# Kernel tuning notes

Measured on AMD Instinct MI355X. Metric: run time of the kernel, lower is better.

## Reference

```python
import jax, jax.numpy as jnp
import numpy as np

N, C, H, W = 4, 256, 64, 64
C_EMBED = C // 2  # 128

def setup_inputs() -> dict:
    key = jax.random.key(0)
    k1, k2, k3, k4 = jax.random.split(key, 4)
    x = jax.random.normal(k1, (N, C, H, W), dtype=jnp.float32)
    # 1x1 conv weights stored as [out_ch, in_ch] (torch Conv2d weight squeezed)
    theta_w = jax.random.normal(k2, (C_EMBED, C), dtype=jnp.float32) * 0.01
    phi_w = jax.random.normal(k3, (C_EMBED, C), dtype=jnp.float32) * 0.01
    proj_w = jax.random.normal(k4, (C, C), dtype=jnp.float32) * 0.01
    return {"x": x, "theta_w": theta_w, "phi_w": phi_w, "proj_w": proj_w}

def reference(x, theta_w, phi_w, proj_w):
    n, c, h, w = x.shape
    s = h * w
    xf = x.reshape(n, c, s)  # [n, c, s]
    theta = jnp.einsum('ec,ncs->nse', theta_w, xf)  # [n, s, e]
    phi = jnp.einsum('ec,ncs->nes', phi_w, xf)      # [n, e, s]
    scale = jnp.sqrt(jnp.float32(theta_w.shape[0]))
    f = jnp.einsum('nse,net->nst', theta, phi) / scale  # [n, s, s]
    f = jax.nn.softmax(f, axis=-1)
    y = jnp.einsum('nst,nct->ncs', f, xf)  # attend over g = x, -> [n, c, s]
    res = jnp.einsum('oc,ncs->nos', proj_w, y)  # 1x1 projection conv
    return x + res.reshape(n, c, h, w)
```

## Files before the change

kernel.cpp:

```cpp
#include <hip/hip_runtime.h>
#include <cstdint>
#include <cstddef>

#define NB 4
#define CH 256
#define SS 4096
#define EE 128
#define QSCALE 0.08838834764831845f

typedef __attribute__((ext_vector_type(8))) short bfrag;
typedef __attribute__((ext_vector_type(8))) unsigned short u16x8;
typedef __attribute__((ext_vector_type(4))) float f32x4;

__device__ __forceinline__ unsigned short f2bf(float f) {
  union { float f; unsigned int u; } v; v.f = f;
  unsigned int u = v.u;
  unsigned int r = u + 0x7FFFu + ((u >> 16) & 1u);
  return (unsigned short)(r >> 16);
}

__global__ __launch_bounds__(256) void cvt_all(
    const float* __restrict__ x,   const float* __restrict__ thw,
    const float* __restrict__ phw, const float* __restrict__ pw,
    unsigned short* __restrict__ xb,   unsigned short* __restrict__ thwb,
    unsigned short* __restrict__ phwb, unsigned short* __restrict__ pwb)
{
  const int nx4 = NB * CH * SS / 4;
  const int nw4 = EE * CH / 4;
  const int np4 = CH * CH / 4;
  int i = blockIdx.x * 256 + threadIdx.x;
  const float* src; unsigned short* dst; int off;
  if      (i < nx4)                 { src = x;   dst = xb;   off = i; }
  else if (i < nx4 + nw4)           { src = thw; dst = thwb; off = i - nx4; }
  else if (i < nx4 + 2 * nw4)       { src = phw; dst = phwb; off = i - nx4 - nw4; }
  else if (i < nx4 + 2 * nw4 + np4) { src = pw;  dst = pwb;  off = i - nx4 - 2 * nw4; }
  else return;
  float4 v = reinterpret_cast<const float4*>(src)[off];
  ushort4 o;
  o.x = f2bf(v.x); o.y = f2bf(v.y); o.z = f2bf(v.z); o.w = f2bf(v.w);
  reinterpret_cast<ushort4*>(dst)[off] = o;
}

__global__ __launch_bounds__(256) void pass1_qk(
    const unsigned short* __restrict__ xb,
    const unsigned short* __restrict__ thw,
    const unsigned short* __restrict__ phw,
    unsigned short* __restrict__ Qt,
    unsigned short* __restrict__ Kt)
{
  __shared__ unsigned short xT[64][CH + 8];
  const int t  = threadIdx.x;
  const int n  = blockIdx.y;
  const int s0 = blockIdx.x * 64;
  const int z  = blockIdx.z;

  {
    const int soff = (t & 15) * 4;
    const int c0   = t >> 4;
    const ushort4* xv = reinterpret_cast<const ushort4*>(
        xb + ((size_t)n * CH) * SS + s0);
    #pragma unroll
    for (int ci = 0; ci < 16; ++ci) {
      const int c = c0 + ci * 16;
      ushort4 v = xv[c * (SS / 4) + (soff >> 2)];
      xT[soff + 0][c] = v.x;
      xT[soff + 1][c] = v.y;
      xT[soff + 2][c] = v.z;
      xT[soff + 3][c] = v.w;
    }
  }
  __syncthreads();

  const int w    = t >> 6;
  const int lane = t & 63;
  const int q    = lane >> 4;
  const int mr   = lane & 15;

  bfrag a[8];
  {
    const bfrag* rp = reinterpret_cast<const bfrag*>(&xT[w * 16 + mr][0]);
    #pragma unroll
    for (int k = 0; k < 8; ++k) a[k] = rp[k * 4 + q];
  }

  const unsigned short* wsel = z ? phw : thw;
  unsigned short*       osel = z ? Kt  : Qt;
  const float           sc   = z ? 1.0f : QSCALE;
  const bfrag* wp = reinterpret_cast<const bfrag*>(wsel);
  #pragma unroll
  for (int nt = 0; nt < 8; ++nt) {
    f32x4 acc = {0.f, 0.f, 0.f, 0.f};
    #pragma unroll
    for (int k = 0; k < 8; ++k) {
      bfrag b = wp[(nt * 16 + mr) * (CH / 8) + k * 4 + q];
      acc = __builtin_amdgcn_mfma_f32_16x16x32_bf16(a[k], b, acc, 0, 0, 0);
    }
    #pragma unroll
    for (int i = 0; i < 4; ++i) {
      const int srow = s0 + w * 16 + q * 4 + i;
      osel[((size_t)n * SS + srow) * EE + nt * 16 + mr] = f2bf(acc[i] * sc);
    }
  }
}

__global__ __launch_bounds__(512, 2) void pass2_attn(
    const unsigned short* __restrict__ Qt,
    const unsigned short* __restrict__ Kt,
    const unsigned short* __restrict__ xb,
    unsigned short* __restrict__ Yt)
{
  __shared__ float          S_lds[64][132];
  __shared__ unsigned short P_lds[64][136];
  __shared__ float row_m[64], row_l[64], row_alpha[64];

  const int t    = threadIdx.x;
  const int id   = blockIdx.x;
  const int xcd  = id & 7;
  const int n    = xcd >> 1;
  const int s0   = ((id >> 3) * 2 + (xcd & 1)) * 64;
  const int w    = t >> 6;
  const int lane = t & 63;
  const int q    = lane >> 4;
  const int mr   = lane & 15;

  if (t < 64) { row_m[t] = -INFINITY; row_l[t] = 0.f; }

  bfrag qa[4][4];
  #pragma unroll
  for (int ms = 0; ms < 4; ++ms) {
    const bfrag* rp = reinterpret_cast<const bfrag*>(
        Qt + ((size_t)n * SS + s0 + ms * 16 + mr) * EE);
    #pragma unroll
    for (int k = 0; k < 4; ++k) qa[ms][k] = rp[k * 4 + q];
  }

  f32x4 o_acc[4][2];
  #pragma unroll
  for (int ms = 0; ms < 4; ++ms)
    #pragma unroll
    for (int nt = 0; nt < 2; ++nt) o_acc[ms][nt] = (f32x4){0.f, 0.f, 0.f, 0.f};

  bfrag kb[4];
  {
    const bfrag* rp = reinterpret_cast<const bfrag*>(
        Kt + ((size_t)n * SS + w * 16 + mr) * EE);
    #pragma unroll
    for (int k = 0; k < 4; ++k) kb[k] = rp[k * 4 + q];
  }

  for (int t0 = 0; t0 < SS; t0 += 128) {
    bfrag vb[4][2];
    #pragma unroll
    for (int nt = 0; nt < 2; ++nt) {
      const int c = w * 32 + nt * 16 + mr;
      const bfrag* vp = reinterpret_cast<const bfrag*>(
          xb + ((size_t)n * CH + c) * SS + t0);
      #pragma unroll
      for (int kk = 0; kk < 4; ++kk) vb[kk][nt] = vp[kk * 4 + q];
    }

    #pragma unroll
    for (int ms = 0; ms < 4; ++ms) {
      f32x4 acc = {0.f, 0.f, 0.f, 0.f};
      #pragma unroll
      for (int k = 0; k < 4; ++k)
        acc = __builtin_amdgcn_mfma_f32_16x16x32_bf16(qa[ms][k], kb[k], acc, 0, 0, 0);
      #pragma unroll
      for (int i = 0; i < 4; ++i)
        S_lds[ms * 16 + q * 4 + i][w * 16 + mr] = acc[i];
    }
    __syncthreads();

    {
      const int t1 = t0 + 128;
      if (t1 < SS) {
        const bfrag* rp = reinterpret_cast<const bfrag*>(
            Kt + ((size_t)n * SS + t1 + w * 16 + mr) * EE);
        #pragma unroll
        for (int k = 0; k < 4; ++k) kb[k] = rp[k * 4 + q];
      }
    }

    {
      const int r  = t >> 3;
      const int cg = t & 7;
      const float4* srow = reinterpret_cast<const float4*>(&S_lds[r][cg * 16]);
      float4 v0 = srow[0], v1 = srow[1], v2 = srow[2], v3 = srow[3];
      float vmax = fmaxf(fmaxf(fmaxf(v0.x, v0.y), fmaxf(v0.z, v0.w)),
                         fmaxf(fmaxf(v1.x, v1.y), fmaxf(v1.z, v1.w)));
      vmax = fmaxf(vmax, fmaxf(fmaxf(fmaxf(v2.x, v2.y), fmaxf(v2.z, v2.w)),
                               fmaxf(fmaxf(v3.x, v3.y), fmaxf(v3.z, v3.w))));
      vmax = fmaxf(vmax, __shfl_xor(vmax, 1, 8));
      vmax = fmaxf(vmax, __shfl_xor(vmax, 2, 8));
      vmax = fmaxf(vmax, __shfl_xor(vmax, 4, 8));
      const float m_old = row_m[r];
      const float m_new = fmaxf(m_old, vmax);

      float p[16];
      p[0]=__expf(v0.x-m_new); p[1]=__expf(v0.y-m_new); p[2]=__expf(v0.z-m_new); p[3]=__expf(v0.w-m_new);
      p[4]=__expf(v1.x-m_new); p[5]=__expf(v1.y-m_new); p[6]=__expf(v1.z-m_new); p[7]=__expf(v1.w-m_new);
      p[8]=__expf(v2.x-m_new); p[9]=__expf(v2.y-m_new); p[10]=__expf(v2.z-m_new); p[11]=__expf(v2.w-m_new);
      p[12]=__expf(v3.x-m_new); p[13]=__expf(v3.y-m_new); p[14]=__expf(v3.z-m_new); p[15]=__expf(v3.w-m_new);
      float sum = 0.f;
      u16x8 pk0, pk1;
      #pragma unroll
      for (int j = 0; j < 8; ++j) { sum += p[j];     pk0[j] = f2bf(p[j]); }
      #pragma unroll
      for (int j = 0; j < 8; ++j) { sum += p[8 + j]; pk1[j] = f2bf(p[8 + j]); }
      *reinterpret_cast<u16x8*>(&P_lds[r][cg * 16])     = pk0;
      *reinterpret_cast<u16x8*>(&P_lds[r][cg * 16 + 8]) = pk1;
      sum += __shfl_xor(sum, 1, 8);
      sum += __shfl_xor(sum, 2, 8);
      sum += __shfl_xor(sum, 4, 8);
      if (cg == 0) {
        const float al = __expf(m_old - m_new);
        row_alpha[r] = al;
        row_m[r]     = m_new;
        row_l[r]     = row_l[r] * al + sum;
      }
    }
    __syncthreads();

    #pragma unroll
    for (int ms = 0; ms < 4; ++ms) {
      float al[4];
      #pragma unroll
      for (int i = 0; i < 4; ++i) al[i] = row_alpha[ms * 16 + q * 4 + i];
      #pragma unroll
      for (int nt = 0; nt < 2; ++nt)
        #pragma unroll
        for (int i = 0; i < 4; ++i) o_acc[ms][nt][i] *= al[i];
    }

    #pragma unroll
    for (int kk = 0; kk < 4; ++kk) {
      bfrag pa[4];
      #pragma unroll
      for (int ms = 0; ms < 4; ++ms)
        pa[ms] = reinterpret_cast<const bfrag*>(&P_lds[ms * 16 + mr][0])[kk * 4 + q];
      #pragma unroll
      for (int nt = 0; nt < 2; ++nt)
        #pragma unroll
        for (int ms = 0; ms < 4; ++ms)
          o_acc[ms][nt] = __builtin_amdgcn_mfma_f32_16x16x32_bf16(
              pa[ms], vb[kk][nt], o_acc[ms][nt], 0, 0, 0);
    }
  }

  #pragma unroll
  for (int ms = 0; ms < 4; ++ms) {
    float inv[4];
    #pragma unroll
    for (int i = 0; i < 4; ++i) inv[i] = 1.0f / row_l[ms * 16 + q * 4 + i];
    #pragma unroll
    for (int nt = 0; nt < 2; ++nt) {
      const int c = w * 32 + nt * 16 + mr;
      #pragma unroll
      for (int i = 0; i < 4; ++i) {
        const int s = s0 + ms * 16 + q * 4 + i;
        Yt[((size_t)n * SS + s) * CH + c] = f2bf(o_acc[ms][nt][i] * inv[i]);
      }
    }
  }
}

__global__ __launch_bounds__(256) void pass3_proj(
    const unsigned short* __restrict__ Yt,
    const unsigned short* __restrict__ pw,
    const float* __restrict__ x,
    float* __restrict__ out)
{
  const int t    = threadIdx.x;
  const int w    = t >> 6;
  const int lane = t & 63;
  const int q    = lane >> 4;
  const int mr   = lane & 15;
  const int n    = blockIdx.z;
  const int o0   = blockIdx.y * 64 + w * 16;
  const int s1   = blockIdx.x * 64;

  bfrag a[8];
  {
    const bfrag* ap = reinterpret_cast<const bfrag*>(pw + (o0 + mr) * CH);
    #pragma unroll
    for (int k = 0; k < 8; ++k) a[k] = ap[k * 4 + q];
  }

  #pragma unroll
  for (int nt = 0; nt < 4; ++nt) {
    f32x4 acc = {0.f, 0.f, 0.f, 0.f};
    const bfrag* bp = reinterpret_cast<const bfrag*>(
        Yt + ((size_t)n * SS + s1 + nt * 16 + mr) * CH);
    #pragma unroll
    for (int k = 0; k < 8; ++k)
      acc = __builtin_amdgcn_mfma_f32_16x16x32_bf16(a[k], bp[k * 4 + q], acc, 0, 0, 0);
    #pragma unroll
    for (int i = 0; i < 4; ++i) {
      const int o = o0 + q * 4 + i;
      const int s = s1 + nt * 16 + mr;
      const size_t idx = ((size_t)n * CH + o) * SS + s;
      out[idx] = x[idx] + acc[i];
    }
  }
}

extern "C" void kernel_launch(void* const* d_in, const int* in_sizes, int n_in,
                              void* d_out, int out_size, void* d_ws, size_t ws_size,
                              hipStream_t stream) {
  const float* x   = (const float*)d_in[0];
  const float* thw = (const float*)d_in[1];
  const float* phw = (const float*)d_in[2];
  const float* pw  = (const float*)d_in[3];
  float* out = (float*)d_out;

  unsigned short* xb   = (unsigned short*)d_ws;
  unsigned short* Yt   = xb + (size_t)NB * CH * SS;
  unsigned short* Qt   = Yt + (size_t)NB * CH * SS;
  unsigned short* Kt   = Qt + (size_t)NB * SS * EE;
  unsigned short* thwb = Kt + (size_t)NB * SS * EE;
  unsigned short* phwb = thwb + EE * CH;
  unsigned short* pwb  = phwb + EE * CH;

  const int nx4 = NB * CH * SS / 4;
  const int nw4 = EE * CH / 4;
  const int np4 = CH * CH / 4;
  const int tot4 = nx4 + 2 * nw4 + np4;
  cvt_all<<<(tot4 + 255) / 256, 256, 0, stream>>>(
      x, thw, phw, pw, xb, thwb, phwb, pwb);

  pass1_qk  <<<dim3(SS / 64, NB, 2),       256, 0, stream>>>(xb, thwb, phwb, Qt, Kt);
  pass2_attn<<<dim3(NB * SS / 64),         512, 0, stream>>>(Qt, Kt, xb, Yt);
  pass3_proj<<<dim3(SS / 64, CH / 64, NB), 256, 0, stream>>>(Yt, pwb, x, out);
}
```

Measured before the change: 213.8 us.

## Fuse x conversion into QK projection and output projection into attention

The fp32-to-bf16 conversion of x moves into the Q/K projection kernel. That kernel now computes Q and K in one 512-thread block that shares the transposed x tile, instead of two blocks over a z dimension. The 1x1 output projection plus residual add moves into the attention kernel's epilogue, which stages the normalized Y tile in reused shared memory. This removes two launches and the Yt round trip through global memory, and x is loaded once for both Q and K. In exchange, the attention kernel gains a serial projection tail and more register pressure.

```diff
diff --git a/kernel.cpp b/kernel.cpp
--- a/kernel.cpp
+++ b/kernel.cpp
@@ -19,21 +19,19 @@
   return (unsigned short)(r >> 16);
 }
 
-__global__ __launch_bounds__(256) void cvt_all(
-    const float* __restrict__ x,   const float* __restrict__ thw,
-    const float* __restrict__ phw, const float* __restrict__ pw,
-    unsigned short* __restrict__ xb,   unsigned short* __restrict__ thwb,
-    unsigned short* __restrict__ phwb, unsigned short* __restrict__ pwb)
+__global__ __launch_bounds__(256) void cvt_w(
+    const float* __restrict__ thw, const float* __restrict__ phw,
+    const float* __restrict__ pw,
+    unsigned short* __restrict__ thwb, unsigned short* __restrict__ phwb,
+    unsigned short* __restrict__ pwb)
 {
-  const int nx4 = NB * CH * SS / 4;
   const int nw4 = EE * CH / 4;
   const int np4 = CH * CH / 4;
   int i = blockIdx.x * 256 + threadIdx.x;
   const float* src; unsigned short* dst; int off;
-  if      (i < nx4)                 { src = x;   dst = xb;   off = i; }
-  else if (i < nx4 + nw4)           { src = thw; dst = thwb; off = i - nx4; }
-  else if (i < nx4 + 2 * nw4)       { src = phw; dst = phwb; off = i - nx4 - nw4; }
-  else if (i < nx4 + 2 * nw4 + np4) { src = pw;  dst = pwb;  off = i - nx4 - 2 * nw4; }
+  if      (i < nw4)           { src = thw; dst = thwb; off = i; }
+  else if (i < 2 * nw4)       { src = phw; dst = phwb; off = i - nw4; }
+  else if (i < 2 * nw4 + np4) { src = pw;  dst = pwb;  off = i - 2 * nw4; }
   else return;
   float4 v = reinterpret_cast<const float4*>(src)[off];
   ushort4 o;
@@ -41,10 +39,11 @@
   reinterpret_cast<ushort4*>(dst)[off] = o;
 }
 
-__global__ __launch_bounds__(256) void pass1_qk(
-    const unsigned short* __restrict__ xb,
+__global__ __launch_bounds__(512) void pass1_qk(
+    const float* __restrict__ x,
     const unsigned short* __restrict__ thw,
     const unsigned short* __restrict__ phw,
+    unsigned short* __restrict__ xb,
     unsigned short* __restrict__ Qt,
     unsigned short* __restrict__ Kt)
 {
@@ -52,21 +51,22 @@
   const int t  = threadIdx.x;
   const int n  = blockIdx.y;
   const int s0 = blockIdx.x * 64;
-  const int z  = blockIdx.z;
 
   {
     const int soff = (t & 15) * 4;
     const int c0   = t >> 4;
-    const ushort4* xv = reinterpret_cast<const ushort4*>(
-        xb + ((size_t)n * CH) * SS + s0);
-    #pragma unroll
-    for (int ci = 0; ci < 16; ++ci) {
-      const int c = c0 + ci * 16;
-      ushort4 v = xv[c * (SS / 4) + (soff >> 2)];
-      xT[soff + 0][c] = v.x;
-      xT[soff + 1][c] = v.y;
-      xT[soff + 2][c] = v.z;
-      xT[soff + 3][c] = v.w;
+    #pragma unroll
+    for (int ci = 0; ci < 8; ++ci) {
+      const int c = c0 + ci * 32;
+      const size_t rowoff = ((size_t)n * CH + c) * SS + s0;
+      float4 v = reinterpret_cast<const float4*>(x + rowoff)[soff >> 2];
+      ushort4 o;
+      o.x = f2bf(v.x); o.y = f2bf(v.y); o.z = f2bf(v.z); o.w = f2bf(v.w);
+      reinterpret_cast<ushort4*>(xb + rowoff)[soff >> 2] = o;
+      xT[soff + 0][c] = o.x;
+      xT[soff + 1][c] = o.y;
+      xT[soff + 2][c] = o.z;
+      xT[soff + 3][c] = o.w;
     }
   }
   __syncthreads();
@@ -75,17 +75,19 @@
   const int lane = t & 63;
   const int q    = lane >> 4;
   const int mr   = lane & 15;
+  const int wrow = (w & 3) * 16;
+  const int half = w >> 2;
 
   bfrag a[8];
   {
-    const bfrag* rp = reinterpret_cast<const bfrag*>(&xT[w * 16 + mr][0]);
+    const bfrag* rp = reinterpret_cast<const bfrag*>(&xT[wrow + mr][0]);
     #pragma unroll
     for (int k = 0; k < 8; ++k) a[k] = rp[k * 4 + q];
   }
 
-  const unsigned short* wsel = z ? phw : thw;
-  unsigned short*       osel = z ? Kt  : Qt;
-  const float           sc   = z ? 1.0f : QSCALE;
+  const unsigned short* wsel = half ? phw : thw;
+  unsigned short*       osel = half ? Kt  : Qt;
+  const float           sc   = half ? 1.0f : QSCALE;
   const bfrag* wp = reinterpret_cast<const bfrag*>(wsel);
   #pragma unroll
   for (int nt = 0; nt < 8; ++nt) {
@@ -97,7 +99,7 @@
     }
     #pragma unroll
     for (int i = 0; i < 4; ++i) {
-      const int srow = s0 + w * 16 + q * 4 + i;
+      const int srow = s0 + wrow + q * 4 + i;
       osel[((size_t)n * SS + srow) * EE + nt * 16 + mr] = f2bf(acc[i] * sc);
     }
   }
@@ -107,11 +109,16 @@
     const unsigned short* __restrict__ Qt,
     const unsigned short* __restrict__ Kt,
     const unsigned short* __restrict__ xb,
-    unsigned short* __restrict__ Yt)
+    const unsigned short* __restrict__ pwb,
+    const float* __restrict__ x,
+    float* __restrict__ out)
 {
-  __shared__ float          S_lds[64][132];
-  __shared__ unsigned short P_lds[64][136];
-  __shared__ float row_m[64], row_l[64], row_alpha[64];
+  __shared__ __align__(16) unsigned char SMEM[51968];
+  float          (*S_lds)[132] = reinterpret_cast<float(*)[132]>(SMEM);
+  unsigned short (*P_lds)[136] = reinterpret_cast<unsigned short(*)[136]>(SMEM + 33792);
+  float* row_m     = reinterpret_cast<float*>(SMEM + 51200);
+  float* row_l     = reinterpret_cast<float*>(SMEM + 51456);
+  float* row_alpha = reinterpret_cast<float*>(SMEM + 51712);
 
   const int t    = threadIdx.x;
   const int id   = blockIdx.x;
@@ -247,6 +254,10 @@
     }
   }
 
+  __syncthreads();
+  unsigned short (*Y_lds)[CH + 8] =
+      reinterpret_cast<unsigned short(*)[CH + 8]>(SMEM);
+
   #pragma unroll
   for (int ms = 0; ms < 4; ++ms) {
     float inv[4];
@@ -256,50 +267,35 @@
     for (int nt = 0; nt < 2; ++nt) {
       const int c = w * 32 + nt * 16 + mr;
       #pragma unroll
+      for (int i = 0; i < 4; ++i)
+        Y_lds[ms * 16 + q * 4 + i][c] = f2bf(o_acc[ms][nt][i] * inv[i]);
+    }
+  }
+  __syncthreads();
+
+  #pragma unroll
+  for (int ot = 0; ot < 2; ++ot) {
+    const int o0 = w * 32 + ot * 16;
+    bfrag a[8];
+    {
+      const bfrag* ap = reinterpret_cast<const bfrag*>(pwb + (o0 + mr) * CH);
+      #pragma unroll
+      for (int k = 0; k < 8; ++k) a[k] = ap[k * 4 + q];
+    }
+    #pragma unroll
+    for (int st = 0; st < 4; ++st) {
+      f32x4 acc = {0.f, 0.f, 0.f, 0.f};
+      const bfrag* bp = reinterpret_cast<const bfrag*>(&Y_lds[st * 16 + mr][0]);
+      #pragma unroll
+      for (int k = 0; k < 8; ++k)
+        acc = __builtin_amdgcn_mfma_f32_16x16x32_bf16(a[k], bp[k * 4 + q], acc, 0, 0, 0);
+      #pragma unroll
       for (int i = 0; i < 4; ++i) {
-        const int s = s0 + ms * 16 + q * 4 + i;
-        Yt[((size_t)n * SS + s) * CH + c] = f2bf(o_acc[ms][nt][i] * inv[i]);
+        const int o = o0 + q * 4 + i;
+        const int s = s0 + st * 16 + mr;
+        const size_t idx = ((size_t)n * CH + o) * SS + s;
+        out[idx] = x[idx] + acc[i];
       }
-    }
-  }
-}
-
-__global__ __launch_bounds__(256) void pass3_proj(
-    const unsigned short* __restrict__ Yt,
-    const unsigned short* __restrict__ pw,
-    const float* __restrict__ x,
-    float* __restrict__ out)
-{
-  const int t    = threadIdx.x;
-  const int w    = t >> 6;
-  const int lane = t & 63;
-  const int q    = lane >> 4;
-  const int mr   = lane & 15;
-  const int n    = blockIdx.z;
-  const int o0   = blockIdx.y * 64 + w * 16;
-  const int s1   = blockIdx.x * 64;
-
-  bfrag a[8];
-  {
-    const bfrag* ap = reinterpret_cast<const bfrag*>(pw + (o0 + mr) * CH);
-    #pragma unroll
-    for (int k = 0; k < 8; ++k) a[k] = ap[k * 4 + q];
-  }
-
-  #pragma unroll
-  for (int nt = 0; nt < 4; ++nt) {
-    f32x4 acc = {0.f, 0.f, 0.f, 0.f};
-    const bfrag* bp = reinterpret_cast<const bfrag*>(
-        Yt + ((size_t)n * SS + s1 + nt * 16 + mr) * CH);
-    #pragma unroll
-    for (int k = 0; k < 8; ++k)
-      acc = __builtin_amdgcn_mfma_f32_16x16x32_bf16(a[k], bp[k * 4 + q], acc, 0, 0, 0);
-    #pragma unroll
-    for (int i = 0; i < 4; ++i) {
-      const int o = o0 + q * 4 + i;
-      const int s = s1 + nt * 16 + mr;
-      const size_t idx = ((size_t)n * CH + o) * SS + s;
-      out[idx] = x[idx] + acc[i];
     }
   }
 }
@@ -314,21 +310,17 @@
   float* out = (float*)d_out;
 
   unsigned short* xb   = (unsigned short*)d_ws;
-  unsigned short* Yt   = xb + (size_t)NB * CH * SS;
-  unsigned short* Qt   = Yt + (size_t)NB * CH * SS;
+  unsigned short* Qt   = xb + (size_t)NB * CH * SS;
   unsigned short* Kt   = Qt + (size_t)NB * SS * EE;
   unsigned short* thwb = Kt + (size_t)NB * SS * EE;
   unsigned short* phwb = thwb + EE * CH;
   unsigned short* pwb  = phwb + EE * CH;
 
-  const int nx4 = NB * CH * SS / 4;
   const int nw4 = EE * CH / 4;
   const int np4 = CH * CH / 4;
-  const int tot4 = nx4 + 2 * nw4 + np4;
-  cvt_all<<<(tot4 + 255) / 256, 256, 0, stream>>>(
-      x, thw, phw, pw, xb, thwb, phwb, pwb);
-
-  pass1_qk  <<<dim3(SS / 64, NB, 2),       256, 0, stream>>>(xb, thwb, phwb, Qt, Kt);
-  pass2_attn<<<dim3(NB * SS / 64),         512, 0, stream>>>(Qt, Kt, xb, Yt);
-  pass3_proj<<<dim3(SS / 64, CH / 64, NB), 256, 0, stream>>>(Yt, pwb, x, out);
-}
+  const int totw4 = 2 * nw4 + np4;
+  cvt_w<<<(totw4 + 255) / 256, 256, 0, stream>>>(thw, phw, pw, thwb, phwb, pwb);
+
+  pass1_qk  <<<dim3(SS / 64, NB), 512, 0, stream>>>(x, thwb, phwb, xb, Qt, Kt);
+  pass2_attn<<<dim3(NB * SS / 64), 512, 0, stream>>>(Qt, Kt, xb, pwb, x, out);
+}
```

After: 196.4 us. 8.1% less time.
